# Kernel tuning notes

Hardware: AMD Instinct MI355X
Metric: run time of the kernel (lower is better)

The kernel has to match this reference:

```python
import jax, jax.numpy as jnp
import numpy as np

B, T, I, H, O = 256, 128, 2048, 128, 2


def setup_inputs() -> dict:
    key = jax.random.key(0)
    ks = jax.random.split(key, 5)
    return {
        "x": jax.random.normal(ks[0], (B, T, I), dtype=jnp.float32),
        "Wi": jax.random.normal(ks[1], (I, 4 * H), dtype=jnp.float32) / np.sqrt(I),
        "Uh": jax.random.normal(ks[2], (H, 4 * H), dtype=jnp.float32) / np.sqrt(H),
        "b": jnp.zeros((4 * H,), dtype=jnp.float32),
        "Wout": jax.random.normal(ks[3], (H, O), dtype=jnp.float32) / np.sqrt(H),
        "bout": jnp.zeros((O,), dtype=jnp.float32),
    }


def reference(x, Wi, Uh, b, Wout, bout):
    # x: [B, T, I] -> reshape(-1, T, I) is identity here
    Bx, Tx = x.shape[0], x.shape[1]
    Hh = Uh.shape[0]
    # precompute input contributions for all timesteps: [B, T, 4H]
    xg = jnp.einsum('bti,ig->btg', x, Wi)
    c0 = jnp.zeros((Bx, Hh), dtype=x.dtype)
    h0 = jnp.zeros((Bx, Hh), dtype=x.dtype)

    def step(carry, xt):
        c, h = carry
        z = xt + h @ Uh + b  # [B, 4H], flax gate order: i, f, g, o
        i, f, g, o = jnp.split(z, 4, axis=-1)
        c_new = jax.nn.sigmoid(f) * c + jax.nn.sigmoid(i) * jnp.tanh(g)
        h_new = jax.nn.sigmoid(o) * jnp.tanh(c_new)
        return (c_new, h_new), None

    (c_f, h_f), _ = jax.lax.scan(step, (c0, h0), jnp.swapaxes(xg, 0, 1))
    # final hidden state -> dense output head
    return h_f @ Wout + bout
```

## Files before the change

### kernel.cpp

```cpp
#include <hip/hip_runtime.h>
#include <stdint.h>

#define B_ 256
#define T_ 128
#define I_ 2048
#define H_ 128
#define G_ 512
#define O_ 2

typedef _Float16 half8 __attribute__((ext_vector_type(8)));
typedef float f32x4 __attribute__((ext_vector_type(4)));

__device__ __forceinline__ void gll16(const void* g, void* l) {
    __builtin_amdgcn_global_load_lds((const __attribute__((address_space(1))) unsigned int*)g,
                                     (__attribute__((address_space(3))) unsigned int*)l,
                                     16, 0, 0);
}

__global__ void wt2(const float* __restrict__ Wi, _Float16* __restrict__ Wt) {
    __shared__ float tile[32][33];
    const int k0 = (blockIdx.x >> 4) * 32;
    const int n0 = (blockIdx.x & 15) * 32;
    const int t = threadIdx.x;
    const int r = t >> 5, c = t & 31;
    #pragma unroll
    for (int i = 0; i < 4; ++i)
        tile[r + 8 * i][c] = Wi[(size_t)(k0 + r + 8 * i) * G_ + n0 + c];
    __syncthreads();
    #pragma unroll
    for (int i = 0; i < 4; ++i)
        Wt[(size_t)(n0 + r + 8 * i) * I_ + k0 + c] = (_Float16)tile[c][r + 8 * i];
}

__launch_bounds__(256, 3)
__global__ void gemm_xg(const float* __restrict__ X, const _Float16* __restrict__ Wt,
                        _Float16* __restrict__ xg) {
    __shared__ float    lds_a[2][128 * 32];
    __shared__ _Float16 lds_b[2][128 * 32];

    const int bid = blockIdx.x;
    const int swz = (bid & 7) * 128 + (bid >> 3);
    const int m0 = (swz >> 2) * 128;
    const int n0 = (swz & 3) * 128;

    const int tid = threadIdx.x;
    const int l = tid & 63, w = tid >> 6;
    const int wm = w >> 1, wn = w & 1;
    const int lr = l & 15;
    const int q  = l >> 4;

    const int a_unit = (l & 7) ^ (l >> 3);
    const float* aglb = X + (size_t)(m0 + w * 32 + (l >> 3)) * I_ + a_unit * 4;
    const int b_r4 = (l >> 2) & 3;
    const int b_r2 = (l >> 4) & 3;
    const int b_unit = (l & 3) ^ ((b_r4 + b_r2) & 3);
    const _Float16* bglb = Wt + (size_t)(n0 + w * 32 + (l >> 2)) * I_ + b_unit * 8;

    f32x4 acc[4][4];
    #pragma unroll
    for (int mi = 0; mi < 4; ++mi)
        #pragma unroll
        for (int ni = 0; ni < 4; ++ni)
            acc[mi][ni] = (f32x4){0.f, 0.f, 0.f, 0.f};

    #pragma unroll
    for (int cc = 0; cc < 4; ++cc)
        gll16(aglb + (size_t)cc * 8 * I_, (char*)&lds_a[0][0] + (w * 4 + cc) * 1024);
    #pragma unroll
    for (int cc = 0; cc < 2; ++cc)
        gll16(bglb + (size_t)cc * 16 * I_, (char*)&lds_b[0][0] + (w * 2 + cc) * 1024);
    __syncthreads();

    for (int kt = 0; kt < I_ / 32; ++kt) {
        const int cur = kt & 1;
        if (kt < I_ / 32 - 1) {
            const int ko = (kt + 1) * 32;
            #pragma unroll
            for (int cc = 0; cc < 4; ++cc)
                gll16(aglb + ko + (size_t)cc * 8 * I_,
                      (char*)&lds_a[cur ^ 1][0] + (w * 4 + cc) * 1024);
            #pragma unroll
            for (int cc = 0; cc < 2; ++cc)
                gll16(bglb + ko + (size_t)cc * 16 * I_,
                      (char*)&lds_b[cur ^ 1][0] + (w * 2 + cc) * 1024);
        }

        half8 af[4], bf[4];
        #pragma unroll
        for (int mi = 0; mi < 4; ++mi) {
            const int row = wm * 64 + mi * 16 + lr;
            const int plo = (2 * q) ^ (row & 7);
            const int phi = plo ^ 1;
            f32x4 lo = *(const f32x4*)&lds_a[cur][row * 32 + plo * 4];
            f32x4 hi = *(const f32x4*)&lds_a[cur][row * 32 + phi * 4];
            half8 h;
            h[0]=(_Float16)lo[0]; h[1]=(_Float16)lo[1]; h[2]=(_Float16)lo[2]; h[3]=(_Float16)lo[3];
            h[4]=(_Float16)hi[0]; h[5]=(_Float16)hi[1]; h[6]=(_Float16)hi[2]; h[7]=(_Float16)hi[3];
            af[mi] = h;
        }
        #pragma unroll
        for (int ni = 0; ni < 4; ++ni) {
            const int row = wn * 64 + ni * 16 + lr;
            const int fB = ((row & 3) + ((row >> 2) & 3)) & 3;
            bf[ni] = *(const half8*)&lds_b[cur][row * 32 + (q ^ fB) * 8];
        }
        #pragma unroll
        for (int mi = 0; mi < 4; ++mi)
            #pragma unroll
            for (int ni = 0; ni < 4; ++ni)
                acc[mi][ni] = __builtin_amdgcn_mfma_f32_16x16x32_f16(af[mi], bf[ni], acc[mi][ni], 0, 0, 0);

        __syncthreads();
    }

    #pragma unroll
    for (int mi = 0; mi < 4; ++mi) {
        #pragma unroll
        for (int ni = 0; ni < 4; ++ni) {
            const int col = n0 + wn * 64 + ni * 16 + lr;
            #pragma unroll
            for (int r = 0; r < 4; ++r) {
                const int row = m0 + wm * 64 + mi * 16 + q * 4 + r;
                xg[(size_t)row * G_ + col] = (_Float16)acc[mi][ni][r];
            }
        }
    }
}

__device__ __forceinline__ float sigmoidf_fast(float x) {
    return 1.f / (1.f + __expf(-x));
}
__device__ __forceinline__ float tanhf_fast(float x) {
    return 1.f - 2.f / (__expf(2.f * x) + 1.f);
}

__launch_bounds__(512, 2)
__global__ void lstm_scan(const _Float16* __restrict__ xg, const float* __restrict__ Uh,
                          const float* __restrict__ bias, const float* __restrict__ Wout,
                          const float* __restrict__ bout, float* __restrict__ out) {
    __shared__ float h4[2][4][36];
    const int t = threadIdx.x;
    const int w = t >> 6, l = t & 63;
    const int lr = l & 15, p = l >> 4;
    const int j = w * 16 + lr;

    float U[32][4];
    #pragma unroll
    for (int m = 0; m < 32; ++m)
        #pragma unroll
        for (int c = 0; c < 4; ++c)
            U[m][c] = Uh[(size_t)(32 * p + m) * G_ + j + 128 * c];
    float bj[4];
    #pragma unroll
    for (int c = 0; c < 4; ++c) bj[c] = bias[j + 128 * c];

    for (int idx = t; idx < 2 * 4 * 36; idx += 512) ((float*)h4)[idx] = 0.f;

    const _Float16* xgb = xg + (size_t)blockIdx.x * T_ * G_;
    float xv[4], xn[4] = {0.f, 0.f, 0.f, 0.f};
    #pragma unroll
    for (int c = 0; c < 4; ++c) xv[c] = (float)xgb[j + 128 * c];
    float cst = 0.f;
    const int wslice = w >> 1;
    const float seed = (p == 0) ? 1.f : 0.f;
    __syncthreads();

    for (int tt = 0; tt < T_; ++tt) {
        const int rb = tt & 1;
        if (tt < T_ - 1) {
            #pragma unroll
            for (int c = 0; c < 4; ++c) xn[c] = (float)xgb[(size_t)(tt + 1) * G_ + j + 128 * c];
        }
        float z0 = seed * (xv[0] + bj[0]), z1 = seed * (xv[1] + bj[1]);
        float z2 = seed * (xv[2] + bj[2]), z3 = seed * (xv[3] + bj[3]);
        #pragma unroll
        for (int i = 0; i < 8; ++i) {
            f32x4 hv = *(const f32x4*)&h4[rb][p][i * 4];
            #pragma unroll
            for (int mm = 0; mm < 4; ++mm) {
                const float hk = hv[mm];
                z0 += hk * U[i * 4 + mm][0];
                z1 += hk * U[i * 4 + mm][1];
                z2 += hk * U[i * 4 + mm][2];
                z3 += hk * U[i * 4 + mm][3];
            }
        }
        z0 += __shfl_xor(z0, 16); z0 += __shfl_xor(z0, 32);
        z1 += __shfl_xor(z1, 16); z1 += __shfl_xor(z1, 32);
        z2 += __shfl_xor(z2, 16); z2 += __shfl_xor(z2, 32);
        z3 += __shfl_xor(z3, 16); z3 += __shfl_xor(z3, 32);
        const float si = sigmoidf_fast(z0);
        const float sf = sigmoidf_fast(z1);
        const float tg = tanhf_fast(z2);
        const float so = sigmoidf_fast(z3);
        cst = sf * cst + si * tg;
        const float hn = so * tanhf_fast(cst);
        if (p == wslice) h4[rb ^ 1][p][j & 31] = hn;
        #pragma unroll
        for (int c = 0; c < 4; ++c) xv[c] = xn[c];
        __syncthreads();
    }

    if (t < O_) {
        float a0 = 0.f, a1 = 0.f, a2 = 0.f, a3 = 0.f;
        for (int k = 0; k < H_; k += 4) {
            a0 += h4[0][(k + 0) >> 5][(k + 0) & 31] * Wout[(k + 0) * O_ + t];
            a1 += h4[0][(k + 1) >> 5][(k + 1) & 31] * Wout[(k + 1) * O_ + t];
            a2 += h4[0][(k + 2) >> 5][(k + 2) & 31] * Wout[(k + 2) * O_ + t];
            a3 += h4[0][(k + 3) >> 5][(k + 3) & 31] * Wout[(k + 3) * O_ + t];
        }
        out[blockIdx.x * O_ + t] = a0 + a1 + a2 + a3 + bout[t];
    }
}

extern "C" void kernel_launch(void* const* d_in, const int* in_sizes, int n_in,
                              void* d_out, int out_size, void* d_ws, size_t ws_size,
                              hipStream_t stream) {
    const float* x    = (const float*)d_in[0];
    const float* Wi   = (const float*)d_in[1];
    const float* Uh   = (const float*)d_in[2];
    const float* bias = (const float*)d_in[3];
    const float* Wout = (const float*)d_in[4];
    const float* bout = (const float*)d_in[5];
    float* out = (float*)d_out;

    _Float16* Wt = (_Float16*)d_ws;
    _Float16* xg = (_Float16*)((char*)d_ws + (size_t)G_ * I_ * sizeof(_Float16));

    wt2<<<1024, 256, 0, stream>>>(Wi, Wt);
    gemm_xg<<<(B_ * T_ / 128) * (G_ / 128), 256, 0, stream>>>(x, Wt, xg);
    lstm_scan<<<B_, 512, 0, stream>>>(xg, Uh, bias, Wout, bout, out);
}
```

Before: 669.0 us.

## Replace LDS-staged GEMM loads with direct global-to-register fragment loads

The input-projection GEMM no longer stages X and Wt tiles through double-buffered LDS via global_load_lds. Each wave now loads its MFMA fragments straight from global memory into registers, relying on L1/L2 caching for reuse across waves, and drops the per-iteration barriers. The fp32-to-fp16 conversion uses packed cvt_pkrtz, and occupancy hint drops from 3 to 2 blocks. In exchange, operands that were shared through LDS are now re-fetched from cache by each wave, and the strided per-lane loads are less coalesced.

```diff
diff --git a/kernel.cpp b/kernel.cpp
--- a/kernel.cpp
+++ b/kernel.cpp
@@ -9,12 +9,11 @@
 #define O_ 2
 
 typedef _Float16 half8 __attribute__((ext_vector_type(8)));
+typedef _Float16 half2v __attribute__((ext_vector_type(2)));
 typedef float f32x4 __attribute__((ext_vector_type(4)));
 
-__device__ __forceinline__ void gll16(const void* g, void* l) {
-    __builtin_amdgcn_global_load_lds((const __attribute__((address_space(1))) unsigned int*)g,
-                                     (__attribute__((address_space(3))) unsigned int*)l,
-                                     16, 0, 0);
+__device__ __forceinline__ half2v cvt_pk(float a, float b) {
+    return __builtin_bit_cast(half2v, __builtin_amdgcn_cvt_pkrtz(a, b));
 }
 
 __global__ void wt2(const float* __restrict__ Wi, _Float16* __restrict__ Wt) {
@@ -32,12 +31,9 @@
         Wt[(size_t)(n0 + r + 8 * i) * I_ + k0 + c] = (_Float16)tile[c][r + 8 * i];
 }
 
-__launch_bounds__(256, 3)
+__launch_bounds__(256, 2)
 __global__ void gemm_xg(const float* __restrict__ X, const _Float16* __restrict__ Wt,
                         _Float16* __restrict__ xg) {
-    __shared__ float    lds_a[2][128 * 32];
-    __shared__ _Float16 lds_b[2][128 * 32];
-
     const int bid = blockIdx.x;
     const int swz = (bid & 7) * 128 + (bid >> 3);
     const int m0 = (swz >> 2) * 128;
@@ -49,12 +45,8 @@
     const int lr = l & 15;
     const int q  = l >> 4;
 
-    const int a_unit = (l & 7) ^ (l >> 3);
-    const float* aglb = X + (size_t)(m0 + w * 32 + (l >> 3)) * I_ + a_unit * 4;
-    const int b_r4 = (l >> 2) & 3;
-    const int b_r2 = (l >> 4) & 3;
-    const int b_unit = (l & 3) ^ ((b_r4 + b_r2) & 3);
-    const _Float16* bglb = Wt + (size_t)(n0 + w * 32 + (l >> 2)) * I_ + b_unit * 8;
+    const float*    ap = X  + (size_t)(m0 + wm * 64 + lr) * I_ + q * 8;
+    const _Float16* bp = Wt + (size_t)(n0 + wn * 64 + lr) * I_ + q * 8;
 
     f32x4 acc[4][4];
     #pragma unroll
@@ -63,54 +55,31 @@
         for (int ni = 0; ni < 4; ++ni)
             acc[mi][ni] = (f32x4){0.f, 0.f, 0.f, 0.f};
 
-    #pragma unroll
-    for (int cc = 0; cc < 4; ++cc)
-        gll16(aglb + (size_t)cc * 8 * I_, (char*)&lds_a[0][0] + (w * 4 + cc) * 1024);
-    #pragma unroll
-    for (int cc = 0; cc < 2; ++cc)
-        gll16(bglb + (size_t)cc * 16 * I_, (char*)&lds_b[0][0] + (w * 2 + cc) * 1024);
-    __syncthreads();
-
-    for (int kt = 0; kt < I_ / 32; ++kt) {
-        const int cur = kt & 1;
-        if (kt < I_ / 32 - 1) {
-            const int ko = (kt + 1) * 32;
-            #pragma unroll
-            for (int cc = 0; cc < 4; ++cc)
-                gll16(aglb + ko + (size_t)cc * 8 * I_,
-                      (char*)&lds_a[cur ^ 1][0] + (w * 4 + cc) * 1024);
-            #pragma unroll
-            for (int cc = 0; cc < 2; ++cc)
-                gll16(bglb + ko + (size_t)cc * 16 * I_,
-                      (char*)&lds_b[cur ^ 1][0] + (w * 2 + cc) * 1024);
-        }
-
+    #pragma unroll 2
+    for (int kk = 0; kk < I_; kk += 32) {
         half8 af[4], bf[4];
         #pragma unroll
         for (int mi = 0; mi < 4; ++mi) {
-            const int row = wm * 64 + mi * 16 + lr;
-            const int plo = (2 * q) ^ (row & 7);
-            const int phi = plo ^ 1;
-            f32x4 lo = *(const f32x4*)&lds_a[cur][row * 32 + plo * 4];
-            f32x4 hi = *(const f32x4*)&lds_a[cur][row * 32 + phi * 4];
+            const float* p = ap + (size_t)mi * 16 * I_ + kk;
+            f32x4 lo = *(const f32x4*)p;
+            f32x4 hi = *(const f32x4*)(p + 4);
+            half2v h0 = cvt_pk(lo[0], lo[1]);
+            half2v h1 = cvt_pk(lo[2], lo[3]);
+            half2v h2 = cvt_pk(hi[0], hi[1]);
+            half2v h3 = cvt_pk(hi[2], hi[3]);
             half8 h;
-            h[0]=(_Float16)lo[0]; h[1]=(_Float16)lo[1]; h[2]=(_Float16)lo[2]; h[3]=(_Float16)lo[3];
-            h[4]=(_Float16)hi[0]; h[5]=(_Float16)hi[1]; h[6]=(_Float16)hi[2]; h[7]=(_Float16)hi[3];
+            h[0]=h0[0]; h[1]=h0[1]; h[2]=h1[0]; h[3]=h1[1];
+            h[4]=h2[0]; h[5]=h2[1]; h[6]=h3[0]; h[7]=h3[1];
             af[mi] = h;
         }
         #pragma unroll
-        for (int ni = 0; ni < 4; ++ni) {
-            const int row = wn * 64 + ni * 16 + lr;
-            const int fB = ((row & 3) + ((row >> 2) & 3)) & 3;
-            bf[ni] = *(const half8*)&lds_b[cur][row * 32 + (q ^ fB) * 8];
-        }
+        for (int ni = 0; ni < 4; ++ni)
+            bf[ni] = *(const half8*)(bp + (size_t)ni * 16 * I_ + kk);
         #pragma unroll
         for (int mi = 0; mi < 4; ++mi)
             #pragma unroll
             for (int ni = 0; ni < 4; ++ni)
                 acc[mi][ni] = __builtin_amdgcn_mfma_f32_16x16x32_f16(af[mi], bf[ni], acc[mi][ni], 0, 0, 0);
-
-        __syncthreads();
     }
 
     #pragma unroll
```

Measured after the change: 769.6 us. 15.0% more time.
